# Optimization experiments

Hardware: AMD Instinct MI355X
Metric: run time of the kernel (lower is better)

The kernel has to match this reference:

```python
import jax, jax.numpy as jnp
import numpy as np

BATCH_SIZE_PER_IM = 512
FG_FRACTION = 0.25
FG_THRESH = 0.5
BG_THRESH_HI = 0.5
BG_THRESH_LO = 0.0
MAX_FG = int(FG_FRACTION * BATCH_SIZE_PER_IM)  # 128


def _rand_boxes(key, shape):
    a = jax.random.uniform(key, shape + (4,), dtype=jnp.float32)
    ymin = jnp.minimum(a[..., 0], a[..., 2])
    ymax = jnp.maximum(a[..., 0], a[..., 2]) + 1e-3
    xmin = jnp.minimum(a[..., 1], a[..., 3])
    xmax = jnp.maximum(a[..., 1], a[..., 3]) + 1e-3
    return jnp.stack([ymin, xmin, ymax, xmax], axis=-1)


def setup_inputs() -> dict:
    key = jax.random.key(0)
    k1, k2, k3, k4 = jax.random.split(key, 4)
    B, N, G = 32, 8192, 128
    boxes = _rand_boxes(k1, (B, N))
    gt_boxes = _rand_boxes(k2, (B, G))
    gt_labels = jax.random.randint(k3, (B, G), 0, 91, dtype=jnp.int32)
    noise = jax.random.uniform(k4, (B, N + G), dtype=jnp.float32)
    return {"boxes": boxes, "gt_boxes": gt_boxes, "gt_labels": gt_labels, "noise": noise}


def _bbox_overlap(boxes, gt_boxes):
    # boxes: [B, M, 4], gt_boxes: [B, G, 4], layout (ymin, xmin, ymax, xmax)
    b_ymin, b_xmin, b_ymax, b_xmax = [boxes[..., i:i + 1] for i in range(4)]  # [B,M,1]
    g_ymin, g_xmin, g_ymax, g_xmax = [gt_boxes[..., i][:, None, :] for i in range(4)]  # [B,1,G]
    i_ymin = jnp.maximum(b_ymin, g_ymin)
    i_xmin = jnp.maximum(b_xmin, g_xmin)
    i_ymax = jnp.minimum(b_ymax, g_ymax)
    i_xmax = jnp.minimum(b_xmax, g_xmax)
    i_area = jnp.maximum(i_ymax - i_ymin, 0.0) * jnp.maximum(i_xmax - i_xmin, 0.0)  # [B,M,G]
    b_area = (b_ymax - b_ymin) * (b_xmax - b_xmin)           # [B,M,1]
    g_area = (g_ymax - g_ymin) * (g_xmax - g_xmin)           # [B,1,G]
    iou = i_area / (b_area + g_area - i_area)
    # padded gt boxes (filled with -1) get IoU = -1
    padding = jnp.logical_and(i_ymin < 0, i_xmin < 0)
    return jnp.where(padding, -1.0, iou)


def reference(boxes, gt_boxes, gt_labels, noise):
    boxes = jax.lax.stop_gradient(boxes)
    all_boxes = jnp.concatenate([boxes, gt_boxes], axis=1)        # [B, M=N+G, 4]
    iou = _bbox_overlap(all_boxes, gt_boxes)                      # [B, M, G]
    max_ov = jnp.max(iou, axis=2)                                 # [B, M]
    p2l = jnp.argmax(iou, axis=2).astype(jnp.int32)               # [B, M]
    box_t = jnp.take_along_axis(gt_boxes, p2l[..., None], axis=1)  # [B, M, 4]
    cls_t = jnp.take_along_axis(gt_labels, p2l, axis=1)           # [B, M]
    pos = max_ov > FG_THRESH
    neg = jnp.logical_and(max_ov >= BG_THRESH_LO, max_ov < BG_THRESH_HI)
    cls_t = jnp.where(neg, 0, cls_t)
    box_t = jnp.where(neg[..., None], 0.0, box_t)
    p2l = jnp.where(neg, 0, p2l)
    # --- balanced fg/bg subsampling (random scores provided in `noise`) ---
    pos_score = jnp.where(pos, noise, -1.0)
    kth = jax.lax.top_k(pos_score, MAX_FG)[0][:, -1:]             # [B,1] threshold
    sel_pos = jnp.logical_and(pos, pos_score >= kth)              # at most MAX_FG fg
    # selected fg get priority band 2+, bg band [0,1), rest -1
    combined = jnp.where(sel_pos, 2.0 + noise, jnp.where(neg, noise, -1.0))
    _, idx = jax.lax.top_k(combined, BATCH_SIZE_PER_IM)           # [B, K]
    rois = jnp.take_along_axis(all_boxes, idx[..., None], axis=1)      # [B, K, 4]
    sample_box_t = jnp.take_along_axis(box_t, idx[..., None], axis=1)  # [B, K, 4]
    sample_cls_t = jnp.take_along_axis(cls_t, idx, axis=1)             # [B, K]
    sample_p2l = jnp.take_along_axis(p2l, idx, axis=1)                 # [B, K]
    return sample_box_t, sample_cls_t, rois, sample_p2l
```

## Files before the change

### kernel.cpp

```cpp
#include <hip/hip_runtime.h>
#include <stdint.h>

#define BATCH 32
#define NBOX 8192
#define NGT 128
#define M (NBOX + NGT)
#define K_OUT 512
#define MAX_FG 128
#define C_CAP 256
#define S_CAP 256
#define U_CAP 1024

#define GSPLIT 2
#define GPER (NGT / GSPLIT)
#define IOU_TPB 256
#define IOU_CB ((M + IOU_TPB - 1) / IOU_TPB)

__device__ __forceinline__ unsigned int bkt1024(float ns) {
    unsigned int u = (unsigned int)(ns * 16777216.0f) >> 14;
    return u > 1023u ? 1023u : u;
}

#define U64KEY(lo, hi) (((unsigned long long)(hi) << 32) | (unsigned long long)(lo))

__global__ __launch_bounds__(256) void iou_kernel(
    const float* __restrict__ boxes,
    const float* __restrict__ gt_boxes,
    unsigned long long* __restrict__ part)
{
    const int s  = blockIdx.x % GSPLIT;
    const int cb = (blockIdx.x / GSPLIT) % IOU_CB;
    const int b  = blockIdx.x / (GSPLIT * IOU_CB);
    const int t  = threadIdx.x;
    const int g0 = s * GPER;

    __shared__ float4 sgt[GPER];
    __shared__ float  sga[GPER];
    if (t < GPER) {
        float4 g = ((const float4*)gt_boxes)[b * NGT + g0 + t];
        sgt[t] = g;
        sga[t] = __fmul_rn(__fsub_rn(g.z, g.x), __fsub_rn(g.w, g.y));
    }
    __syncthreads();

    const int m = cb * IOU_TPB + t;
    if (m >= M) return;

    float4 bb = (m < NBOX) ? ((const float4*)boxes)[b * NBOX + m]
                           : ((const float4*)gt_boxes)[b * NGT + (m - NBOX)];
    float ba = __fmul_rn(__fsub_rn(bb.z, bb.x), __fsub_rn(bb.w, bb.y));

    float best = -1e30f;
    int bi = 0;
    #pragma unroll 4
    for (int g = 0; g < GPER; ++g) {
        float4 gg = sgt[g];
        float iymin = fmaxf(bb.x, gg.x);
        float ixmin = fmaxf(bb.y, gg.y);
        float iymax = fminf(bb.z, gg.z);
        float ixmax = fminf(bb.w, gg.w);
        float ia  = __fmul_rn(fmaxf(__fsub_rn(iymax, iymin), 0.0f),
                              fmaxf(__fsub_rn(ixmax, ixmin), 0.0f));
        float den = __fsub_rn(__fadd_rn(ba, sga[g]), ia);
        float iou = __fdiv_rn(ia, den);
        if (iou > best) { best = iou; bi = g0 + g; }
    }
    part[((size_t)s * BATCH + b) * M + m] =
        U64KEY(127u - (unsigned int)bi, __float_as_uint(best));
}

__global__ __launch_bounds__(1024) void select_kernel(
    const float* __restrict__ boxes,
    const float* __restrict__ gt_boxes,
    const int*   __restrict__ gt_labels,
    const float* __restrict__ noise,
    const unsigned long long* __restrict__ part,
    float* __restrict__ out)
{
    const int b = blockIdx.x;
    const int tid = threadIdx.x;

    __shared__ float sh_ns[M];
    __shared__ unsigned char sh_idx[M];
    __shared__ unsigned int hist[1024];
    __shared__ unsigned int hist2[1024];
    __shared__ unsigned int bctr[1024];
    __shared__ unsigned char posmask[M / 8];
    __shared__ unsigned char negmask[M / 8];
    __shared__ float4 sgt[NGT];
    __shared__ int slab[NGT];
    __shared__ float C[C_CAP];
    __shared__ __align__(16) unsigned int   skey[S_CAP + 4];
    __shared__ __align__(16) unsigned short sm[S_CAP + 4];
    __shared__ unsigned int   ukey[U_CAP];
    __shared__ unsigned short um[U_CAP];
    __shared__ unsigned int sh_Bp, sh_needp, sh_cc, sh_n1a, sh_B, sh_kth;

    float* out_bt  = out;
    float* out_cls = out + BATCH * K_OUT * 4;
    float* out_roi = out + BATCH * K_OUT * 5;
    float* out_p2l = out + BATCH * K_OUT * 9;

    hist[tid] = 0;
    hist2[tid] = 0;
    bctr[tid] = 0;
    if (tid == 0) { sh_cc = 0; sh_n1a = 0; sh_B = 0; sh_kth = 0xBF800000u; }
    if (tid < NGT) {
        sgt[tid]  = ((const float4*)gt_boxes)[b * NGT + tid];
        slab[tid] = gt_labels[b * NGT + tid];
    }
    __syncthreads();

    float f[8];
    unsigned int pb = 0, nb = 0;
    {
        const unsigned long long* P0 = part + ((size_t)0 * BATCH + b) * M;
        const unsigned long long* P1 = part + ((size_t)1 * BATCH + b) * M;
        const float4* ns4 = (const float4*)(noise + (size_t)b * M);
        {
            const int c = tid;
            const uint4* a4 = (const uint4*)(P0 + (size_t)c * 8);
            const uint4* b4 = (const uint4*)(P1 + (size_t)c * 8);
            uint4 A0 = a4[0], A1 = a4[1], A2 = a4[2], A3 = a4[3];
            uint4 B0 = b4[0], B1 = b4[1], B2 = b4[2], B3 = b4[3];
            float4 n0 = ns4[2 * c], n1v = ns4[2 * c + 1];
            ((float4*)sh_ns)[2 * c] = n0;
            ((float4*)sh_ns)[2 * c + 1] = n1v;
            f[0] = n0.x; f[1] = n0.y; f[2] = n0.z; f[3] = n0.w;
            f[4] = n1v.x; f[5] = n1v.y; f[6] = n1v.z; f[7] = n1v.w;
            unsigned long long ka[8] = {
                U64KEY(A0.x, A0.y), U64KEY(A0.z, A0.w),
                U64KEY(A1.x, A1.y), U64KEY(A1.z, A1.w),
                U64KEY(A2.x, A2.y), U64KEY(A2.z, A2.w),
                U64KEY(A3.x, A3.y), U64KEY(A3.z, A3.w)};
            unsigned long long kb[8] = {
                U64KEY(B0.x, B0.y), U64KEY(B0.z, B0.w),
                U64KEY(B1.x, B1.y), U64KEY(B1.z, B1.w),
                U64KEY(B2.x, B2.y), U64KEY(B2.z, B2.w),
                U64KEY(B3.x, B3.y), U64KEY(B3.z, B3.w)};
            #pragma unroll
            for (int k = 0; k < 8; ++k) {
                unsigned long long kk = ka[k] > kb[k] ? ka[k] : kb[k];
                unsigned int ub = (unsigned int)(kk >> 32);
                sh_idx[c * 8 + k] = (unsigned char)(127u - ((unsigned int)kk & 127u));
                if (ub > 0x3F000000u) {
                    pb |= (1u << k);
                    atomicAdd(&hist2[bkt1024(f[k])], 1u);
                } else if (ub < 0x3F000000u) {
                    nb |= (1u << k);
                    atomicAdd(&hist[bkt1024(f[k])], 1u);
                }
            }
            posmask[c] = (unsigned char)pb;
            negmask[c] = (unsigned char)nb;
        }
        if (tid < 16) {
            const int c = 1024 + tid;
            const uint4* a4 = (const uint4*)(P0 + (size_t)c * 8);
            const uint4* b4 = (const uint4*)(P1 + (size_t)c * 8);
            uint4 A0 = a4[0], A1 = a4[1], A2 = a4[2], A3 = a4[3];
            uint4 B0 = b4[0], B1 = b4[1], B2 = b4[2], B3 = b4[3];
            float4 n0 = ns4[2 * c], n1v = ns4[2 * c + 1];
            ((float4*)sh_ns)[2 * c] = n0;
            ((float4*)sh_ns)[2 * c + 1] = n1v;
            float ft[8] = {n0.x, n0.y, n0.z, n0.w, n1v.x, n1v.y, n1v.z, n1v.w};
            unsigned long long ka[8] = {
                U64KEY(A0.x, A0.y), U64KEY(A0.z, A0.w),
                U64KEY(A1.x, A1.y), U64KEY(A1.z, A1.w),
                U64KEY(A2.x, A2.y), U64KEY(A2.z, A2.w),
                U64KEY(A3.x, A3.y), U64KEY(A3.z, A3.w)};
            unsigned long long kb[8] = {
                U64KEY(B0.x, B0.y), U64KEY(B0.z, B0.w),
                U64KEY(B1.x, B1.y), U64KEY(B1.z, B1.w),
                U64KEY(B2.x, B2.y), U64KEY(B2.z, B2.w),
                U64KEY(B3.x, B3.y), U64KEY(B3.z, B3.w)};
            unsigned int pb2 = 0, nb2 = 0;
            #pragma unroll
            for (int k = 0; k < 8; ++k) {
                unsigned long long kk = ka[k] > kb[k] ? ka[k] : kb[k];
                unsigned int ub = (unsigned int)(kk >> 32);
                sh_idx[c * 8 + k] = (unsigned char)(127u - ((unsigned int)kk & 127u));
                if (ub > 0x3F000000u) {
                    pb2 |= (1u << k);
                    atomicAdd(&hist2[bkt1024(ft[k])], 1u);
                } else if (ub < 0x3F000000u) {
                    nb2 |= (1u << k);
                    atomicAdd(&hist[bkt1024(ft[k])], 1u);
                }
            }
            posmask[c] = (unsigned char)pb2;
            negmask[c] = (unsigned char)nb2;
        }
    }
    __syncthreads();

    {
        const int wv = tid >> 6, ln = tid & 63;
        if (wv < 2) {
            unsigned int* H = wv ? hist2 : hist;
            unsigned int s[16];
            #pragma unroll
            for (int k = 0; k < 16; ++k) {
                unsigned int v = H[k * 64 + ln];
                #pragma unroll
                for (int off = 1; off < 64; off <<= 1) {
                    unsigned int o = __shfl_down(v, off, 64);
                    if (ln + off < 64) v += o;
                }
                s[k] = v;
            }
            unsigned int after = 0;
            #pragma unroll
            for (int k = 15; k >= 0; --k) {
                unsigned int tot = __shfl(s[k], 0, 64);
                H[k * 64 + ln] = s[k] + after;
                after += tot;
            }
        }
    }
    __syncthreads();
    const unsigned int nneg = hist[0];
    const unsigned int npos = hist2[0];

    if (npos >= MAX_FG) {
        {
            unsigned int S  = hist2[tid];
            unsigned int Sn = (tid < 1023) ? hist2[tid + 1] : 0;
            if (S >= MAX_FG && Sn < MAX_FG) { sh_Bp = tid; sh_needp = MAX_FG - Sn; }
        }
        __syncthreads();
        const unsigned int Bp = sh_Bp, needp = sh_needp;
        #pragma unroll
        for (int k = 0; k < 8; ++k) {
            if (((pb >> k) & 1u) && bkt1024(f[k]) == Bp) {
                unsigned int slot = atomicAdd(&sh_cc, 1u);
                if (slot < C_CAP) C[slot] = f[k];
            }
        }
        if (tid < 16) {
            unsigned int pb2 = posmask[1024 + tid];
            #pragma unroll
            for (int k = 0; k < 8; ++k) {
                if ((pb2 >> k) & 1u) {
                    float v = sh_ns[(1024 + tid) * 8 + k];
                    if (bkt1024(v) == Bp) {
                        unsigned int slot = atomicAdd(&sh_cc, 1u);
                        if (slot < C_CAP) C[slot] = v;
                    }
                }
            }
        }
        __syncthreads();
        {
            unsigned int cc = min(sh_cc, (unsigned int)C_CAP);
            if (tid < (int)cc) {
                float my = C[tid];
                unsigned int g = 0, e = 0;
                for (unsigned int j = 0; j < cc; ++j) {
                    float v = C[j];
                    g += (v > my) ? 1u : 0u;
                    e += (v == my) ? 1u : 0u;
                }
                if (g < needp && g + e >= needp) sh_kth = __float_as_uint(my);
            }
        }
        __syncthreads();
    }
    const float kthf = __uint_as_float(sh_kth);

    #pragma unroll
    for (int k = 0; k < 8; ++k) {
        if (((pb >> k) & 1u) && f[k] >= kthf) {
            unsigned int slot = atomicAdd(&sh_n1a, 1u);
            if (slot < S_CAP) {
                skey[slot] = __float_as_uint(__fadd_rn(2.0f, f[k]));
                sm[slot]   = (unsigned short)(tid * 8 + k);
            }
        }
    }
    if (tid < 16) {
        unsigned int pb2 = posmask[1024 + tid];
        #pragma unroll
        for (int k = 0; k < 8; ++k) {
            if ((pb2 >> k) & 1u) {
                int m = (1024 + tid) * 8 + k;
                float v = sh_ns[m];
                if (v >= kthf) {
                    unsigned int slot = atomicAdd(&sh_n1a, 1u);
                    if (slot < S_CAP) {
                        skey[slot] = __float_as_uint(__fadd_rn(2.0f, v));
                        sm[slot]   = (unsigned short)m;
                    }
                }
            }
        }
    }
    __syncthreads();
    const unsigned int n1 = min(sh_n1a, (unsigned int)S_CAP);
    const unsigned int k2 = K_OUT - n1;
    const bool enough_neg = (nneg >= k2);

    if (tid < 4) { skey[n1 + tid] = 0u; sm[n1 + tid] = 0xFFFFu; }
    if (enough_neg) {
        unsigned int S  = hist[tid];
        unsigned int Sn = (tid < 1023) ? hist[tid + 1] : 0;
        if (S >= k2 && Sn < k2) sh_B = tid;
    }
    __syncthreads();
    const unsigned int B1 = sh_B;

    if (tid < (int)n1) {
        unsigned int   ki = skey[tid];
        unsigned short mi = sm[tid];
        unsigned int r = 0;
        for (unsigned int j = 0; j < n1; j += 4) {
            uint4   kv = *(const uint4*)&skey[j];
            ushort4 mv = *(const ushort4*)&sm[j];
            r += (kv.x > ki || (kv.x == ki && mv.x < mi)) ? 1u : 0u;
            r += (kv.y > ki || (kv.y == ki && mv.y < mi)) ? 1u : 0u;
            r += (kv.z > ki || (kv.z == ki && mv.z < mi)) ? 1u : 0u;
            r += (kv.w > ki || (kv.w == ki && mv.w < mi)) ? 1u : 0u;
        }
        int mi_ = mi;
        int lbl = sh_idx[mi_];
        float4 roi = (mi_ < NBOX) ? ((const float4*)boxes)[b * NBOX + mi_]
                                  : sgt[mi_ - NBOX];
        ((float4*)out_bt)[b * K_OUT + r] = sgt[lbl];
        out_cls[b * K_OUT + r] = (float)slab[lbl];
        ((float4*)out_roi)[b * K_OUT + r] = roi;
        out_p2l[b * K_OUT + r] = (float)lbl;
    }

    #pragma unroll
    for (int k = 0; k < 8; ++k) {
        if ((nb >> k) & 1u) {
            float v = f[k];
            unsigned int be = bkt1024(v);
            if (be >= B1) {
                unsigned int base = (be < 1023) ? hist[be + 1] : 0;
                unsigned int a = base + atomicAdd(&bctr[be], 1u);
                if (a < U_CAP) {
                    ukey[a] = __float_as_uint(v);
                    um[a]   = (unsigned short)(tid * 8 + k);
                }
            }
        }
    }
    if (tid < 16) {
        unsigned int nb2 = negmask[1024 + tid];
        #pragma unroll
        for (int k = 0; k < 8; ++k) {
            if ((nb2 >> k) & 1u) {
                int m = (1024 + tid) * 8 + k;
                float v = sh_ns[m];
                unsigned int be = bkt1024(v);
                if (be >= B1) {
                    unsigned int base = (be < 1023) ? hist[be + 1] : 0;
                    unsigned int a = base + atomicAdd(&bctr[be], 1u);
                    if (a < U_CAP) {
                        ukey[a] = __float_as_uint(v);
                        um[a]   = (unsigned short)m;
                    }
                }
            }
        }
    }
    __syncthreads();

    const unsigned int q = min(hist[B1], (unsigned int)U_CAP);
    for (unsigned int a = tid; a < q; a += 1024) {
        unsigned int   ki = ukey[a];
        unsigned short mi = um[a];
        unsigned int be = bkt1024(__uint_as_float(ki));
        unsigned int base = (be < 1023) ? hist[be + 1] : 0;
        unsigned int end  = min(hist[be], q);
        unsigned int r = base;
        for (unsigned int j = base; j < end; ++j) {
            unsigned int kj = ukey[j];
            if (kj > ki || (kj == ki && um[j] < mi)) ++r;
        }
        if (r < k2) {
            float4 roi = (mi < NBOX) ? ((const float4*)boxes)[b * NBOX + mi]
                                     : sgt[mi - NBOX];
            unsigned int gr = n1 + r;
            ((float4*)out_bt)[b * K_OUT + gr] = make_float4(0.f, 0.f, 0.f, 0.f);
            out_cls[b * K_OUT + gr] = 0.0f;
            ((float4*)out_roi)[b * K_OUT + gr] = roi;
            out_p2l[b * K_OUT + gr] = 0.0f;
        }
    }

    if (!enough_neg) {
        __syncthreads();
        const unsigned int k3 = k2 - nneg;
        for (int m = tid; m < M; m += 1024) {
            if (((posmask[m >> 3] >> (m & 7)) & 1) && sh_ns[m] < kthf) {
                unsigned int r = 0;
                for (int m2 = 0; m2 < m; ++m2)
                    if (((posmask[m2 >> 3] >> (m2 & 7)) & 1) && sh_ns[m2] < kthf) ++r;
                if (r < k3) {
                    int lbl = sh_idx[m];
                    float4 roi = (m < NBOX) ? ((const float4*)boxes)[b * NBOX + m]
                                            : sgt[m - NBOX];
                    unsigned int gr = n1 + nneg + r;
                    ((float4*)out_bt)[b * K_OUT + gr] = sgt[lbl];
                    out_cls[b * K_OUT + gr] = (float)slab[lbl];
                    ((float4*)out_roi)[b * K_OUT + gr] = roi;
                    out_p2l[b * K_OUT + gr] = (float)lbl;
                }
            }
        }
    }
}

extern "C" void kernel_launch(void* const* d_in, const int* in_sizes, int n_in,
                              void* d_out, int out_size, void* d_ws, size_t ws_size,
                              hipStream_t stream) {
    const float* boxes     = (const float*)d_in[0];
    const float* gt_boxes  = (const float*)d_in[1];
    const int*   gt_labels = (const int*)d_in[2];
    const float* noise     = (const float*)d_in[3];
    unsigned long long* part = (unsigned long long*)d_ws;
    float* out = (float*)d_out;

    iou_kernel<<<BATCH * IOU_CB * GSPLIT, IOU_TPB, 0, stream>>>(boxes, gt_boxes, part);
    select_kernel<<<BATCH, 1024, 0, stream>>>(boxes, gt_boxes, gt_labels, noise,
                                              part, out);
}
```

Measured before the change: 107.2 us.

## Split IoU partials into separate value and label arrays, drop large shared buffers

After: 105.6 us. Within noise of the previous version (-1.5%).

```diff
diff --git a/kernel.cpp b/kernel.cpp
--- a/kernel.cpp
+++ b/kernel.cpp
@@ -16,17 +16,18 @@
 #define IOU_TPB 256
 #define IOU_CB ((M + IOU_TPB - 1) / IOU_TPB)
 
+#define TH_HALF 0x3F000000u
+
 __device__ __forceinline__ unsigned int bkt1024(float ns) {
     unsigned int u = (unsigned int)(ns * 16777216.0f) >> 14;
     return u > 1023u ? 1023u : u;
 }
 
-#define U64KEY(lo, hi) (((unsigned long long)(hi) << 32) | (unsigned long long)(lo))
-
-__global__ __launch_bounds__(256) void iou_kernel(
+__global__ __launch_bounds__(256, 8) void iou_kernel(
     const float* __restrict__ boxes,
     const float* __restrict__ gt_boxes,
-    unsigned long long* __restrict__ part)
+    unsigned int*  __restrict__ Hh,
+    unsigned char* __restrict__ Ll)
 {
     const int s  = blockIdx.x % GSPLIT;
     const int cb = (blockIdx.x / GSPLIT) % IOU_CB;
@@ -65,8 +66,17 @@
         float iou = __fdiv_rn(ia, den);
         if (iou > best) { best = iou; bi = g0 + g; }
     }
-    part[((size_t)s * BATCH + b) * M + m] =
-        U64KEY(127u - (unsigned int)bi, __float_as_uint(best));
+    const size_t o = ((size_t)s * BATCH + b) * M + m;
+    Hh[o] = __float_as_uint(best);
+    Ll[o] = (unsigned char)bi;
+}
+
+__device__ __forceinline__ int merged_label(
+    const unsigned int* __restrict__ H0, const unsigned int* __restrict__ H1,
+    const unsigned char* __restrict__ L0, const unsigned char* __restrict__ L1,
+    int m) {
+    unsigned int h0 = H0[m], h1 = H1[m];
+    return (h0 >= h1) ? (int)L0[m] : (int)L1[m];
 }
 
 __global__ __launch_bounds__(1024) void select_kernel(
@@ -74,14 +84,14 @@
     const float* __restrict__ gt_boxes,
     const int*   __restrict__ gt_labels,
     const float* __restrict__ noise,
-    const unsigned long long* __restrict__ part,
+    const unsigned int*  __restrict__ Hh,
+    const unsigned char* __restrict__ Ll,
     float* __restrict__ out)
 {
     const int b = blockIdx.x;
     const int tid = threadIdx.x;
 
-    __shared__ float sh_ns[M];
-    __shared__ unsigned char sh_idx[M];
+    __shared__ float sh_ns_t[128];
     __shared__ unsigned int hist[1024];
     __shared__ unsigned int hist2[1024];
     __shared__ unsigned int bctr[1024];
@@ -101,6 +111,11 @@
     float* out_roi = out + BATCH * K_OUT * 5;
     float* out_p2l = out + BATCH * K_OUT * 9;
 
+    const unsigned int*  H0 = Hh + (size_t)b * M;
+    const unsigned int*  H1 = Hh + ((size_t)BATCH + b) * M;
+    const unsigned char* L0 = Ll + (size_t)b * M;
+    const unsigned char* L1 = Ll + ((size_t)BATCH + b) * M;
+
     hist[tid] = 0;
     hist2[tid] = 0;
     bctr[tid] = 0;
@@ -114,39 +129,25 @@
     float f[8];
     unsigned int pb = 0, nb = 0;
     {
-        const unsigned long long* P0 = part + ((size_t)0 * BATCH + b) * M;
-        const unsigned long long* P1 = part + ((size_t)1 * BATCH + b) * M;
         const float4* ns4 = (const float4*)(noise + (size_t)b * M);
         {
             const int c = tid;
-            const uint4* a4 = (const uint4*)(P0 + (size_t)c * 8);
-            const uint4* b4 = (const uint4*)(P1 + (size_t)c * 8);
-            uint4 A0 = a4[0], A1 = a4[1], A2 = a4[2], A3 = a4[3];
-            uint4 B0 = b4[0], B1 = b4[1], B2 = b4[2], B3 = b4[3];
+            const uint4* h0v = (const uint4*)(H0 + c * 8);
+            const uint4* h1v = (const uint4*)(H1 + c * 8);
+            uint4 A0 = h0v[0], A1 = h0v[1];
+            uint4 B0 = h1v[0], B1 = h1v[1];
             float4 n0 = ns4[2 * c], n1v = ns4[2 * c + 1];
-            ((float4*)sh_ns)[2 * c] = n0;
-            ((float4*)sh_ns)[2 * c + 1] = n1v;
             f[0] = n0.x; f[1] = n0.y; f[2] = n0.z; f[3] = n0.w;
             f[4] = n1v.x; f[5] = n1v.y; f[6] = n1v.z; f[7] = n1v.w;
-            unsigned long long ka[8] = {
-                U64KEY(A0.x, A0.y), U64KEY(A0.z, A0.w),
-                U64KEY(A1.x, A1.y), U64KEY(A1.z, A1.w),
-                U64KEY(A2.x, A2.y), U64KEY(A2.z, A2.w),
-                U64KEY(A3.x, A3.y), U64KEY(A3.z, A3.w)};
-            unsigned long long kb[8] = {
-                U64KEY(B0.x, B0.y), U64KEY(B0.z, B0.w),
-                U64KEY(B1.x, B1.y), U64KEY(B1.z, B1.w),
-                U64KEY(B2.x, B2.y), U64KEY(B2.z, B2.w),
-                U64KEY(B3.x, B3.y), U64KEY(B3.z, B3.w)};
+            unsigned int ha[8] = {A0.x, A0.y, A0.z, A0.w, A1.x, A1.y, A1.z, A1.w};
+            unsigned int hb[8] = {B0.x, B0.y, B0.z, B0.w, B1.x, B1.y, B1.z, B1.w};
             #pragma unroll
             for (int k = 0; k < 8; ++k) {
-                unsigned long long kk = ka[k] > kb[k] ? ka[k] : kb[k];
-                unsigned int ub = (unsigned int)(kk >> 32);
-                sh_idx[c * 8 + k] = (unsigned char)(127u - ((unsigned int)kk & 127u));
-                if (ub > 0x3F000000u) {
+                unsigned int ub = ha[k] > hb[k] ? ha[k] : hb[k];
+                if (ub > TH_HALF) {
                     pb |= (1u << k);
                     atomicAdd(&hist2[bkt1024(f[k])], 1u);
-                } else if (ub < 0x3F000000u) {
+                } else if (ub < TH_HALF) {
                     nb |= (1u << k);
                     atomicAdd(&hist[bkt1024(f[k])], 1u);
                 }
@@ -156,34 +157,24 @@
         }
         if (tid < 16) {
             const int c = 1024 + tid;
-            const uint4* a4 = (const uint4*)(P0 + (size_t)c * 8);
-            const uint4* b4 = (const uint4*)(P1 + (size_t)c * 8);
-            uint4 A0 = a4[0], A1 = a4[1], A2 = a4[2], A3 = a4[3];
-            uint4 B0 = b4[0], B1 = b4[1], B2 = b4[2], B3 = b4[3];
+            const uint4* h0v = (const uint4*)(H0 + c * 8);
+            const uint4* h1v = (const uint4*)(H1 + c * 8);
+            uint4 A0 = h0v[0], A1 = h0v[1];
+            uint4 B0 = h1v[0], B1 = h1v[1];
             float4 n0 = ns4[2 * c], n1v = ns4[2 * c + 1];
-            ((float4*)sh_ns)[2 * c] = n0;
-            ((float4*)sh_ns)[2 * c + 1] = n1v;
+            ((float4*)sh_ns_t)[2 * tid] = n0;
+            ((float4*)sh_ns_t)[2 * tid + 1] = n1v;
             float ft[8] = {n0.x, n0.y, n0.z, n0.w, n1v.x, n1v.y, n1v.z, n1v.w};
-            unsigned long long ka[8] = {
-                U64KEY(A0.x, A0.y), U64KEY(A0.z, A0.w),
-                U64KEY(A1.x, A1.y), U64KEY(A1.z, A1.w),
-                U64KEY(A2.x, A2.y), U64KEY(A2.z, A2.w),
-                U64KEY(A3.x, A3.y), U64KEY(A3.z, A3.w)};
-            unsigned long long kb[8] = {
-                U64KEY(B0.x, B0.y), U64KEY(B0.z, B0.w),
-                U64KEY(B1.x, B1.y), U64KEY(B1.z, B1.w),
-                U64KEY(B2.x, B2.y), U64KEY(B2.z, B2.w),
-                U64KEY(B3.x, B3.y), U64KEY(B3.z, B3.w)};
+            unsigned int ha[8] = {A0.x, A0.y, A0.z, A0.w, A1.x, A1.y, A1.z, A1.w};
+            unsigned int hb[8] = {B0.x, B0.y, B0.z, B0.w, B1.x, B1.y, B1.z, B1.w};
             unsigned int pb2 = 0, nb2 = 0;
             #pragma unroll
             for (int k = 0; k < 8; ++k) {
-                unsigned long long kk = ka[k] > kb[k] ? ka[k] : kb[k];
-                unsigned int ub = (unsigned int)(kk >> 32);
-                sh_idx[c * 8 + k] = (unsigned char)(127u - ((unsigned int)kk & 127u));
-                if (ub > 0x3F000000u) {
+                unsigned int ub = ha[k] > hb[k] ? ha[k] : hb[k];
+                if (ub > TH_HALF) {
                     pb2 |= (1u << k);
                     atomicAdd(&hist2[bkt1024(ft[k])], 1u);
-                } else if (ub < 0x3F000000u) {
+                } else if (ub < TH_HALF) {
                     nb2 |= (1u << k);
                     atomicAdd(&hist[bkt1024(ft[k])], 1u);
                 }
@@ -242,7 +233,7 @@
             #pragma unroll
             for (int k = 0; k < 8; ++k) {
                 if ((pb2 >> k) & 1u) {
-                    float v = sh_ns[(1024 + tid) * 8 + k];
+                    float v = sh_ns_t[tid * 8 + k];
                     if (bkt1024(v) == Bp) {
                         unsigned int slot = atomicAdd(&sh_cc, 1u);
                         if (slot < C_CAP) C[slot] = v;
@@ -283,13 +274,12 @@
         #pragma unroll
         for (int k = 0; k < 8; ++k) {
             if ((pb2 >> k) & 1u) {
-                int m = (1024 + tid) * 8 + k;
-                float v = sh_ns[m];
+                float v = sh_ns_t[tid * 8 + k];
                 if (v >= kthf) {
                     unsigned int slot = atomicAdd(&sh_n1a, 1u);
                     if (slot < S_CAP) {
                         skey[slot] = __float_as_uint(__fadd_rn(2.0f, v));
-                        sm[slot]   = (unsigned short)m;
+                        sm[slot]   = (unsigned short)((1024 + tid) * 8 + k);
                     }
                 }
             }
@@ -322,7 +312,7 @@
             r += (kv.w > ki || (kv.w == ki && mv.w < mi)) ? 1u : 0u;
         }
         int mi_ = mi;
-        int lbl = sh_idx[mi_];
+        int lbl = merged_label(H0, H1, L0, L1, mi_);
         float4 roi = (mi_ < NBOX) ? ((const float4*)boxes)[b * NBOX + mi_]
                                   : sgt[mi_ - NBOX];
         ((float4*)out_bt)[b * K_OUT + r] = sgt[lbl];
@@ -351,15 +341,14 @@
         #pragma unroll
         for (int k = 0; k < 8; ++k) {
             if ((nb2 >> k) & 1u) {
-                int m = (1024 + tid) * 8 + k;
-                float v = sh_ns[m];
+                float v = sh_ns_t[tid * 8 + k];
                 unsigned int be = bkt1024(v);
                 if (be >= B1) {
                     unsigned int base = (be < 1023) ? hist[be + 1] : 0;
                     unsigned int a = base + atomicAdd(&bctr[be], 1u);
                     if (a < U_CAP) {
                         ukey[a] = __float_as_uint(v);
-                        um[a]   = (unsigned short)m;
+                        um[a]   = (unsigned short)((1024 + tid) * 8 + k);
                     }
                 }
             }
@@ -393,13 +382,14 @@
     if (!enough_neg) {
         __syncthreads();
         const unsigned int k3 = k2 - nneg;
+        const float* nsb = noise + (size_t)b * M;
         for (int m = tid; m < M; m += 1024) {
-            if (((posmask[m >> 3] >> (m & 7)) & 1) && sh_ns[m] < kthf) {
+            if (((posmask[m >> 3] >> (m & 7)) & 1) && nsb[m] < kthf) {
                 unsigned int r = 0;
                 for (int m2 = 0; m2 < m; ++m2)
-                    if (((posmask[m2 >> 3] >> (m2 & 7)) & 1) && sh_ns[m2] < kthf) ++r;
+                    if (((posmask[m2 >> 3] >> (m2 & 7)) & 1) && nsb[m2] < kthf) ++r;
                 if (r < k3) {
-                    int lbl = sh_idx[m];
+                    int lbl = merged_label(H0, H1, L0, L1, m);
                     float4 roi = (m < NBOX) ? ((const float4*)boxes)[b * NBOX + m]
                                             : sgt[m - NBOX];
                     unsigned int gr = n1 + nneg + r;
@@ -420,10 +410,13 @@
     const float* gt_boxes  = (const float*)d_in[1];
     const int*   gt_labels = (const int*)d_in[2];
     const float* noise     = (const float*)d_in[3];
-    unsigned long long* part = (unsigned long long*)d_ws;
     float* out = (float*)d_out;
 
-    iou_kernel<<<BATCH * IOU_CB * GSPLIT, IOU_TPB, 0, stream>>>(boxes, gt_boxes, part);
-    select_kernel<<<BATCH, 1024, 0, stream>>>(boxes, gt_boxes, gt_labels, noise,
-                                              part, out);
+    unsigned int*  Hh = (unsigned int*)d_ws;
+    unsigned char* Ll = (unsigned char*)d_ws + 2129920;
+
+    iou_kernel<<<BATCH * IOU_CB * GSPLIT, IOU_TPB, 0, stream>>>(
+        boxes, gt_boxes, Hh, Ll);
+    select_kernel<<<BATCH, 1024, 0, stream>>>(
+        boxes, gt_boxes, gt_labels, noise, Hh, Ll, out);
 }
```
